# Optimization experiments

Measured on AMD Instinct MI355X. Metric: run time of the kernel, lower is better.

## Reference

```python
import jax, jax.numpy as jnp
import numpy as np

N_NODES = 50000
HIDDEN = 128
N_REL = 9
N_LAYERS = 3
N_EDGES = 600000


def setup_inputs() -> dict:
    key = jax.random.key(0)
    k1, k2, k3, k4, k5 = jax.random.split(key, 5)
    edge_index = jax.random.randint(k1, (2, N_EDGES), 0, N_NODES, dtype=jnp.int64 if jax.config.jax_enable_x64 else jnp.int32)
    edge_type = jax.random.randint(k2, (N_EDGES,), 0, N_REL, dtype=edge_index.dtype)
    embeddings = jax.random.uniform(k3, (N_NODES, HIDDEN), dtype=jnp.float32)
    weights = jax.random.uniform(k4, (N_LAYERS, N_REL, HIDDEN, HIDDEN), dtype=jnp.float32)
    biases = jax.random.uniform(k5, (N_LAYERS, N_REL, HIDDEN), dtype=jnp.float32)
    return {"edge_index": edge_index, "edge_type": edge_type,
            "embeddings": embeddings, "weights": weights, "biases": biases}


def reference(edge_index, edge_type, embeddings, weights, biases):
    # RGCN: per relation r, messages = emb[src] @ W[l,r] + b[l,r], scatter-summed
    # into dest. Equivalent vectorized form: precompute X = emb @ W for all
    # relations ([R,N,E]), then a single gather + segment_sum over edges.
    L = weights.shape[0]
    N = embeddings.shape[0]
    dest = edge_index[0]
    src = edge_index[1]
    out = embeddings
    for l in range(L):
        X = jnp.einsum('ne,ref->rnf', out, weights[l])        # [R, N, E]
        msg = X[edge_type, src] + biases[l][edge_type]        # [num_edges, E]
        hidden = jax.ops.segment_sum(msg, dest, num_segments=N)  # [N, E]
        if l + 1 < L:
            hidden = jax.nn.relu(hidden)
        out = hidden
    return out
```

## Files before the change

kernel.cpp:

```cpp
#include <hip/hip_runtime.h>

#define NNODES 50000
#define HID 128
#define NREL 9
#define NLAYERS 3
#define NEDGES 600000

#define NBINS (NREL * NNODES)
#define SCAN_CHUNK 1024
#define NBLK ((NBINS + SCAN_CHUNK - 1) / SCAN_CHUNK)

#define KTOT (NREL * HID)
#define GM2 64
#define BK 64
#define NCHUNK (KTOT / BK)
#define PITCH 72
#define EPITCH 136

typedef __attribute__((ext_vector_type(8))) short short8;
typedef __attribute__((ext_vector_type(4))) float f32x4;

__device__ __forceinline__ short f2bf(float f) {
    union { float f; unsigned u; } c; c.f = f;
    unsigned r = c.u + 0x7fff + ((c.u >> 16) & 1);
    return (short)(r >> 16);
}
__device__ __forceinline__ float bf2f(short v) {
    return __uint_as_float(((unsigned)(unsigned short)v) << 16);
}


__global__ void hist2_kernel(const int* __restrict__ dst, const int* __restrict__ etype,
                             int* __restrict__ bins) {
    int e = blockIdx.x * blockDim.x + threadIdx.x;
    if (e < NEDGES) {
        int bin = dst[e] * NREL + etype[e];
        atomicAdd(&bins[bin], 1);
    }
}

__global__ __launch_bounds__(256) void scan_pass1(const int* __restrict__ bins,
                                                  int* __restrict__ blocksum) {
    __shared__ int red[256];
    int b = blockIdx.x, t = threadIdx.x;
    int i0 = b * SCAN_CHUNK + t * 4;
    int s = 0;
#pragma unroll
    for (int k = 0; k < 4; k++)
        if (i0 + k < NBINS) s += bins[i0 + k];
    red[t] = s;
    __syncthreads();
    for (int off = 128; off > 0; off >>= 1) {
        if (t < off) red[t] += red[t + off];
        __syncthreads();
    }
    if (t == 0) blocksum[b] = red[0];
}

__global__ __launch_bounds__(512) void scan_pass2(const int* __restrict__ blocksum,
                                                  int* __restrict__ blockoff,
                                                  int* __restrict__ rowptr) {
    __shared__ int s[512];
    int t = threadIdx.x;
    int v = (t < NBLK) ? blocksum[t] : 0;
    s[t] = v;
    __syncthreads();
    for (int off = 1; off < 512; off <<= 1) {
        int x = (t >= off) ? s[t - off] : 0;
        __syncthreads();
        s[t] += x;
        __syncthreads();
    }
    if (t < NBLK) blockoff[t] = s[t] - v;
    if (t == 0) rowptr[NBINS] = NEDGES;
}

__global__ __launch_bounds__(256) void scan_pass3(const int* __restrict__ bins,
                                                  const int* __restrict__ blockoff,
                                                  int* __restrict__ rowptr,
                                                  int* __restrict__ cursor) {
    __shared__ int sc[256];
    int b = blockIdx.x, t = threadIdx.x;
    int i0 = b * SCAN_CHUNK + t * 4;
    int v[4], p[4];
    int s = 0;
#pragma unroll
    for (int k = 0; k < 4; k++) {
        v[k] = (i0 + k < NBINS) ? bins[i0 + k] : 0;
        p[k] = s;
        s += v[k];
    }
    sc[t] = s;
    __syncthreads();
    for (int off = 1; off < 256; off <<= 1) {
        int x = (t >= off) ? sc[t - off] : 0;
        __syncthreads();
        sc[t] += x;
        __syncthreads();
    }
    int base = blockoff[b] + (sc[t] - s);
#pragma unroll
    for (int k = 0; k < 4; k++) {
        if (i0 + k < NBINS) {
            rowptr[i0 + k] = base + p[k];
            cursor[i0 + k] = base + p[k];
        }
    }
}

__global__ void place_kernel(const int* __restrict__ dst, const int* __restrict__ src,
                             const int* __restrict__ etype,
                             int* __restrict__ cursor, int* __restrict__ bsrc) {
    int e = blockIdx.x * blockDim.x + threadIdx.x;
    if (e < NEDGES) {
        int bin = dst[e] * NREL + etype[e];
        int pos = atomicAdd(&cursor[bin], 1);
        bsrc[pos] = src[e];
    }
}


__global__ __launch_bounds__(256) void convert_w(const float* __restrict__ W,
                                                 short* __restrict__ Wt2) {
    int lr = blockIdx.x;
    int l = lr / NREL, r = lr - l * NREL;
    const float* w = W + (size_t)lr * HID * HID;
    short* o = Wt2 + (size_t)l * HID * KTOT;
    int tid = threadIdx.x;
#pragma unroll 4
    for (int i = 0; i < 64; i++) {
        int elem = i * 256 + tid;
        int kk = elem >> 7, n = elem & 127;
        o[(size_t)n * KTOT + r * HID + kk] = f2bf(w[elem]);
    }
}

__global__ __launch_bounds__(256) void convert_emb(const float* __restrict__ E,
                                                   short* __restrict__ Ebf) {
    int gid = blockIdx.x * blockDim.x + threadIdx.x;
    const float* p = E + (size_t)gid * 8;
    float4 v0 = *(const float4*)p;
    float4 v1 = *(const float4*)(p + 4);
    short8 o = {f2bf(v0.x), f2bf(v0.y), f2bf(v0.z), f2bf(v0.w),
                f2bf(v1.x), f2bf(v1.y), f2bf(v1.z), f2bf(v1.w)};
    *(short8*)(Ebf + (size_t)gid * 8) = o;
}


__global__ __launch_bounds__(256) void gather_kernel(const short* __restrict__ Hbf,
                                                     const int* __restrict__ bsrc,
                                                     const int* __restrict__ rowptr,
                                                     short* __restrict__ S) {
    int gid = blockIdx.x * blockDim.x + threadIdx.x;
    int bin = gid >> 3;
    if (bin >= NBINS) return;
    int ck  = gid & 7;
    int rs = rowptr[bin];
    int re = rowptr[bin + 1];
    float a[16];
#pragma unroll
    for (int i = 0; i < 16; i++) a[i] = 0.f;
    for (int j = rs; j < re; j++) {
        int s = bsrc[j];
        const short* hp = Hbf + (size_t)s * HID + ck * 16;
        short8 v0 = *(const short8*)hp;
        short8 v1 = *(const short8*)(hp + 8);
#pragma unroll
        for (int i = 0; i < 8; i++) a[i]     += bf2f(v0[i]);
#pragma unroll
        for (int i = 0; i < 8; i++) a[i + 8] += bf2f(v1[i]);
    }
    short8 o0 = {f2bf(a[0]),  f2bf(a[1]),  f2bf(a[2]),  f2bf(a[3]),
                 f2bf(a[4]),  f2bf(a[5]),  f2bf(a[6]),  f2bf(a[7])};
    short8 o1 = {f2bf(a[8]),  f2bf(a[9]),  f2bf(a[10]), f2bf(a[11]),
                 f2bf(a[12]), f2bf(a[13]), f2bf(a[14]), f2bf(a[15])};
    short* sp = S + (size_t)bin * HID + ck * 16;
    *(short8*)sp       = o0;
    *(short8*)(sp + 8) = o1;
}


__global__ __launch_bounds__(256) void gemm_kernel(const short* __restrict__ S,
                                                   const short* __restrict__ Wt2l,
                                                   const float* __restrict__ Bias,
                                                   const int* __restrict__ rowptr,
                                                   short* __restrict__ HoutBf,
                                                   float* __restrict__ HoutF,
                                                   int last) {
    __shared__ short lds[GM2 * PITCH + HID * PITCH];
    __shared__ int   rp_s[GM2 * NREL + 1];
    __shared__ float bias_s[NREL * HID];
    short* As = lds;
    short* Bs = lds + GM2 * PITCH;

    int tid  = threadIdx.x;
    int wave = tid >> 6, lane = tid & 63;
    int row0 = blockIdx.x * GM2;
    int m0   = wave * 16;
    int lm = lane & 15, lq = lane >> 4;

    int rpbase = row0 * NREL;
    for (int i = tid; i <= GM2 * NREL; i += 256) {
        int g = rpbase + i;
        rp_s[i] = rowptr[(g < NBINS) ? g : NBINS];
    }
    for (int i = tid; i < NREL * HID; i += 256) bias_s[i] = Bias[i];

    int rowL = tid >> 3;
    int ck   = tid & 7;
    int ar0 = row0 + rowL;        if (ar0 > NNODES - 1) ar0 = NNODES - 1;
    int ar1 = row0 + 32 + rowL;   if (ar1 > NNODES - 1) ar1 = NNODES - 1;
    const short* pA0 = S + (size_t)ar0 * KTOT + ck * 8;
    const short* pA1 = S + (size_t)ar1 * KTOT + ck * 8;
    const short* pB0 = Wt2l + (size_t)(rowL      ) * KTOT + ck * 8;
    const short* pB1 = Wt2l + (size_t)(rowL + 32 ) * KTOT + ck * 8;
    const short* pB2 = Wt2l + (size_t)(rowL + 64 ) * KTOT + ck * 8;
    const short* pB3 = Wt2l + (size_t)(rowL + 96 ) * KTOT + ck * 8;

    short8 ra0 = *(const short8*)pA0;
    short8 ra1 = *(const short8*)pA1;
    short8 rb0 = *(const short8*)pB0;
    short8 rb1 = *(const short8*)pB1;
    short8 rb2 = *(const short8*)pB2;
    short8 rb3 = *(const short8*)pB3;

    f32x4 acc[8];
#pragma unroll
    for (int nt = 0; nt < 8; nt++) acc[nt] = (f32x4){0.f, 0.f, 0.f, 0.f};

    for (int kc = 0; kc < NCHUNK; kc++) {
        __syncthreads();
        *(short8*)&As[ rowL       * PITCH + ck * 8] = ra0;
        *(short8*)&As[(rowL + 32) * PITCH + ck * 8] = ra1;
        *(short8*)&Bs[ rowL       * PITCH + ck * 8] = rb0;
        *(short8*)&Bs[(rowL + 32) * PITCH + ck * 8] = rb1;
        *(short8*)&Bs[(rowL + 64) * PITCH + ck * 8] = rb2;
        *(short8*)&Bs[(rowL + 96) * PITCH + ck * 8] = rb3;
        __syncthreads();
        if (kc + 1 < NCHUNK) {
            int off = (kc + 1) * BK;
            ra0 = *(const short8*)(pA0 + off);
            ra1 = *(const short8*)(pA1 + off);
            rb0 = *(const short8*)(pB0 + off);
            rb1 = *(const short8*)(pB1 + off);
            rb2 = *(const short8*)(pB2 + off);
            rb3 = *(const short8*)(pB3 + off);
        }
#pragma unroll
        for (int ks = 0; ks < 2; ks++) {
            short8 af = *(const short8*)&As[(m0 + lm) * PITCH + ks * 32 + lq * 8];
#pragma unroll
            for (int nt = 0; nt < 8; nt++) {
                short8 bf = *(const short8*)&Bs[(nt * 16 + lm) * PITCH + ks * 32 + lq * 8];
                acc[nt] = __builtin_amdgcn_mfma_f32_16x16x32_bf16(af, bf, acc[nt], 0, 0, 0);
            }
        }
    }
    __syncthreads();

    if (!last) {
        short (*Et)[EPITCH] = (short(*)[EPITCH])lds;
#pragma unroll
        for (int reg = 0; reg < 4; reg++) {
            int rl = m0 + lq * 4 + reg;
            float cr[NREL];
#pragma unroll
            for (int r = 0; r < NREL; r++)
                cr[r] = (float)(rp_s[rl * NREL + r + 1] - rp_s[rl * NREL + r]);
#pragma unroll
            for (int nt = 0; nt < 8; nt++) {
                int n = nt * 16 + lm;
                float b = 0.f;
#pragma unroll
                for (int r = 0; r < NREL; r++) b += cr[r] * bias_s[r * HID + n];
                float o = fmaxf(acc[nt][reg] + b, 0.f);
                Et[rl][n] = f2bf(o);
            }
        }
        __syncthreads();
#pragma unroll
        for (int i = 0; i < 4; i++) {
            int p = i * 256 + tid;
            int row = p >> 4, cc = p & 15;
            int d = row0 + row;
            if (d < NNODES)
                *(short8*)(HoutBf + (size_t)d * HID + cc * 8) = *(const short8*)&Et[row][cc * 8];
        }
    } else {
#pragma unroll
        for (int reg = 0; reg < 4; reg++) {
            int rl = m0 + lq * 4 + reg;
            int d  = row0 + rl;
            if (d >= NNODES) continue;
            float cr[NREL];
#pragma unroll
            for (int r = 0; r < NREL; r++)
                cr[r] = (float)(rp_s[rl * NREL + r + 1] - rp_s[rl * NREL + r]);
#pragma unroll
            for (int nt = 0; nt < 8; nt++) {
                int n = nt * 16 + lm;
                float b = 0.f;
#pragma unroll
                for (int r = 0; r < NREL; r++) b += cr[r] * bias_s[r * HID + n];
                HoutF[(size_t)d * HID + n] = acc[nt][reg] + b;
            }
        }
    }
}


extern "C" void kernel_launch(void* const* d_in, const int* in_sizes, int n_in,
                              void* d_out, int out_size, void* d_ws, size_t ws_size,
                              hipStream_t stream) {
    const int*   edge_index = (const int*)d_in[0];
    const int*   etype      = (const int*)d_in[1];
    const float* emb        = (const float*)d_in[2];
    const float* W          = (const float*)d_in[3];
    const float* Bias       = (const float*)d_in[4];
    float*       out        = (float*)d_out;

    const int* dst  = edge_index;
    const int* srcA = edge_index + NEDGES;

    short* Ebf = (short*)d_ws;
    short* Hbf = Ebf + (size_t)NNODES * HID;
    short* S   = Hbf + (size_t)NNODES * HID;
    short* Wt2 = S + (size_t)NNODES * KTOT;
    int*   bsrc     = (int*)(Wt2 + (size_t)NLAYERS * HID * KTOT);
    int*   bins     = bsrc + NEDGES;
    int*   cursor   = bins + NBINS;
    int*   rowptr   = cursor + NBINS;
    int*   blocksum = rowptr + NBINS + 1;
    int*   blockoff = blocksum + NBLK;

    hipMemsetAsync(bins, 0, NBINS * sizeof(int), stream);
    hist2_kernel<<<(NEDGES + 255) / 256, 256, 0, stream>>>(dst, etype, bins);
    scan_pass1<<<NBLK, 256, 0, stream>>>(bins, blocksum);
    scan_pass2<<<1, 512, 0, stream>>>(blocksum, blockoff, rowptr);
    scan_pass3<<<NBLK, 256, 0, stream>>>(bins, blockoff, rowptr, cursor);
    place_kernel<<<(NEDGES + 255) / 256, 256, 0, stream>>>(dst, srcA, etype, cursor, bsrc);
    convert_w<<<NLAYERS * NREL, 256, 0, stream>>>(W, Wt2);
    convert_emb<<<(NNODES * HID / 8) / 256, 256, 0, stream>>>(emb, Ebf);

    const short* Hin = Ebf;
    for (int l = 0; l < NLAYERS; l++) {
        gather_kernel<<<(NBINS * 8 + 255) / 256, 256, 0, stream>>>(Hin, bsrc, rowptr, S);
        const short* Wtl = Wt2 + (size_t)l * HID * KTOT;
        const float* Bl  = Bias + (size_t)l * NREL * HID;
        int last = (l + 1 == NLAYERS);
        gemm_kernel<<<(NNODES + GM2 - 1) / GM2, 256, 0, stream>>>(
            S, Wtl, Bl, rowptr, Hbf, out, last);
        Hin = Hbf;
    }
}
```

Measured before the change: 438.8 us.

## Fuse per-relation gather into GEMM kernel, dropping the intermediate S buffer

```diff
diff --git a/kernel.cpp b/kernel.cpp
--- a/kernel.cpp
+++ b/kernel.cpp
@@ -12,10 +12,7 @@
 
 #define KTOT (NREL * HID)
 #define GM2 64
-#define BK 64
-#define NCHUNK (KTOT / BK)
-#define PITCH 72
-#define EPITCH 136
+#define FPITCH 136
 
 typedef __attribute__((ext_vector_type(8))) short short8;
 typedef __attribute__((ext_vector_type(4))) float f32x4;
@@ -34,7 +31,7 @@
                              int* __restrict__ bins) {
     int e = blockIdx.x * blockDim.x + threadIdx.x;
     if (e < NEDGES) {
-        int bin = dst[e] * NREL + etype[e];
+        int bin = etype[e] * NNODES + dst[e];
         atomicAdd(&bins[bin], 1);
     }
 }
@@ -113,7 +110,7 @@
                              int* __restrict__ cursor, int* __restrict__ bsrc) {
     int e = blockIdx.x * blockDim.x + threadIdx.x;
     if (e < NEDGES) {
-        int bin = dst[e] * NREL + etype[e];
+        int bin = etype[e] * NNODES + dst[e];
         int pos = atomicAdd(&cursor[bin], 1);
         bsrc[pos] = src[e];
     }
@@ -147,134 +144,135 @@
 }
 
 
-__global__ __launch_bounds__(256) void gather_kernel(const short* __restrict__ Hbf,
-                                                     const int* __restrict__ bsrc,
-                                                     const int* __restrict__ rowptr,
-                                                     short* __restrict__ S) {
-    int gid = blockIdx.x * blockDim.x + threadIdx.x;
-    int bin = gid >> 3;
-    if (bin >= NBINS) return;
-    int ck  = gid & 7;
-    int rs = rowptr[bin];
-    int re = rowptr[bin + 1];
-    float a[16];
-#pragma unroll
-    for (int i = 0; i < 16; i++) a[i] = 0.f;
-    for (int j = rs; j < re; j++) {
-        int s = bsrc[j];
-        const short* hp = Hbf + (size_t)s * HID + ck * 16;
-        short8 v0 = *(const short8*)hp;
-        short8 v1 = *(const short8*)(hp + 8);
-#pragma unroll
-        for (int i = 0; i < 8; i++) a[i]     += bf2f(v0[i]);
-#pragma unroll
-        for (int i = 0; i < 8; i++) a[i + 8] += bf2f(v1[i]);
-    }
-    short8 o0 = {f2bf(a[0]),  f2bf(a[1]),  f2bf(a[2]),  f2bf(a[3]),
-                 f2bf(a[4]),  f2bf(a[5]),  f2bf(a[6]),  f2bf(a[7])};
-    short8 o1 = {f2bf(a[8]),  f2bf(a[9]),  f2bf(a[10]), f2bf(a[11]),
-                 f2bf(a[12]), f2bf(a[13]), f2bf(a[14]), f2bf(a[15])};
-    short* sp = S + (size_t)bin * HID + ck * 16;
-    *(short8*)sp       = o0;
-    *(short8*)(sp + 8) = o1;
-}
-
-
-__global__ __launch_bounds__(256) void gemm_kernel(const short* __restrict__ S,
-                                                   const short* __restrict__ Wt2l,
-                                                   const float* __restrict__ Bias,
-                                                   const int* __restrict__ rowptr,
-                                                   short* __restrict__ HoutBf,
-                                                   float* __restrict__ HoutF,
-                                                   int last) {
-    __shared__ short lds[GM2 * PITCH + HID * PITCH];
-    __shared__ int   rp_s[GM2 * NREL + 1];
+__global__ __launch_bounds__(256) void fused_kernel(const short* __restrict__ Hin,
+                                                    const short* __restrict__ Wt2l,
+                                                    const float* __restrict__ Bias,
+                                                    const int* __restrict__ rowptr,
+                                                    const int* __restrict__ bsrc,
+                                                    short* __restrict__ HoutBf,
+                                                    float* __restrict__ HoutF,
+                                                    int last) {
+    __shared__ short As[GM2 * FPITCH];
+    __shared__ int   rp_s[NREL * (GM2 + 1)];
     __shared__ float bias_s[NREL * HID];
-    short* As = lds;
-    short* Bs = lds + GM2 * PITCH;
 
     int tid  = threadIdx.x;
     int wave = tid >> 6, lane = tid & 63;
+    int lm = lane & 15, lq = lane >> 4;
     int row0 = blockIdx.x * GM2;
-    int m0   = wave * 16;
-    int lm = lane & 15, lq = lane >> 4;
-
-    int rpbase = row0 * NREL;
-    for (int i = tid; i <= GM2 * NREL; i += 256) {
-        int g = rpbase + i;
-        rp_s[i] = rowptr[(g < NBINS) ? g : NBINS];
+    int n0   = wave * 32;
+
+    for (int i = tid; i < NREL * (GM2 + 1); i += 256) {
+        int r = i / (GM2 + 1), o = i - r * (GM2 + 1);
+        int d = row0 + o; if (d > NNODES) d = NNODES;
+        rp_s[i] = rowptr[r * NNODES + d];
     }
     for (int i = tid; i < NREL * HID; i += 256) bias_s[i] = Bias[i];
 
-    int rowL = tid >> 3;
-    int ck   = tid & 7;
-    int ar0 = row0 + rowL;        if (ar0 > NNODES - 1) ar0 = NNODES - 1;
-    int ar1 = row0 + 32 + rowL;   if (ar1 > NNODES - 1) ar1 = NNODES - 1;
-    const short* pA0 = S + (size_t)ar0 * KTOT + ck * 8;
-    const short* pA1 = S + (size_t)ar1 * KTOT + ck * 8;
-    const short* pB0 = Wt2l + (size_t)(rowL      ) * KTOT + ck * 8;
-    const short* pB1 = Wt2l + (size_t)(rowL + 32 ) * KTOT + ck * 8;
-    const short* pB2 = Wt2l + (size_t)(rowL + 64 ) * KTOT + ck * 8;
-    const short* pB3 = Wt2l + (size_t)(rowL + 96 ) * KTOT + ck * 8;
-
-    short8 ra0 = *(const short8*)pA0;
-    short8 ra1 = *(const short8*)pA1;
-    short8 rb0 = *(const short8*)pB0;
-    short8 rb1 = *(const short8*)pB1;
-    short8 rb2 = *(const short8*)pB2;
-    short8 rb3 = *(const short8*)pB3;
-
-    f32x4 acc[8];
-#pragma unroll
-    for (int nt = 0; nt < 8; nt++) acc[nt] = (f32x4){0.f, 0.f, 0.f, 0.f};
-
-    for (int kc = 0; kc < NCHUNK; kc++) {
-        __syncthreads();
-        *(short8*)&As[ rowL       * PITCH + ck * 8] = ra0;
-        *(short8*)&As[(rowL + 32) * PITCH + ck * 8] = ra1;
-        *(short8*)&Bs[ rowL       * PITCH + ck * 8] = rb0;
-        *(short8*)&Bs[(rowL + 32) * PITCH + ck * 8] = rb1;
-        *(short8*)&Bs[(rowL + 64) * PITCH + ck * 8] = rb2;
-        *(short8*)&Bs[(rowL + 96) * PITCH + ck * 8] = rb3;
-        __syncthreads();
-        if (kc + 1 < NCHUNK) {
-            int off = (kc + 1) * BK;
-            ra0 = *(const short8*)(pA0 + off);
-            ra1 = *(const short8*)(pA1 + off);
-            rb0 = *(const short8*)(pB0 + off);
-            rb1 = *(const short8*)(pB1 + off);
-            rb2 = *(const short8*)(pB2 + off);
-            rb3 = *(const short8*)(pB3 + off);
-        }
-#pragma unroll
-        for (int ks = 0; ks < 2; ks++) {
-            short8 af = *(const short8*)&As[(m0 + lm) * PITCH + ks * 32 + lq * 8];
-#pragma unroll
-            for (int nt = 0; nt < 8; nt++) {
-                short8 bf = *(const short8*)&Bs[(nt * 16 + lm) * PITCH + ks * 32 + lq * 8];
-                acc[nt] = __builtin_amdgcn_mfma_f32_16x16x32_bf16(af, bf, acc[nt], 0, 0, 0);
-            }
-        }
-    }
+    int grow = tid >> 2;
+    int gcc  = tid & 3;
+
+    f32x4 acc[4][2];
+#pragma unroll
+    for (int a = 0; a < 4; a++)
+#pragma unroll
+        for (int b = 0; b < 2; b++) acc[a][b] = (f32x4){0.f, 0.f, 0.f, 0.f};
+
+    __syncthreads();
+
+    const short* wb = Wt2l + (size_t)(n0 + lm) * KTOT + lq * 8;
+
+    for (int r = 0; r < NREL; r++) {
+        int rs = rp_s[r * (GM2 + 1) + grow];
+        int re = rp_s[r * (GM2 + 1) + grow + 1];
+        float ga[32];
+#pragma unroll
+        for (int i = 0; i < 32; i++) ga[i] = 0.f;
+        int j = rs;
+        while (j + 1 < re) {
+            int s0 = bsrc[j];
+            int s1 = bsrc[j + 1];
+            const short8* h0 = (const short8*)(Hin + (size_t)s0 * HID + gcc * 32);
+            const short8* h1 = (const short8*)(Hin + (size_t)s1 * HID + gcc * 32);
+            short8 a0 = h0[0], a1 = h0[1], a2 = h0[2], a3 = h0[3];
+            short8 b0 = h1[0], b1 = h1[1], b2 = h1[2], b3 = h1[3];
+#pragma unroll
+            for (int i = 0; i < 8; i++) {
+                ga[i]      += bf2f(a0[i]) + bf2f(b0[i]);
+                ga[i + 8]  += bf2f(a1[i]) + bf2f(b1[i]);
+                ga[i + 16] += bf2f(a2[i]) + bf2f(b2[i]);
+                ga[i + 24] += bf2f(a3[i]) + bf2f(b3[i]);
+            }
+            j += 2;
+        }
+        if (j < re) {
+            int s0 = bsrc[j];
+            const short8* h0 = (const short8*)(Hin + (size_t)s0 * HID + gcc * 32);
+            short8 a0 = h0[0], a1 = h0[1], a2 = h0[2], a3 = h0[3];
+#pragma unroll
+            for (int i = 0; i < 8; i++) {
+                ga[i]      += bf2f(a0[i]);
+                ga[i + 8]  += bf2f(a1[i]);
+                ga[i + 16] += bf2f(a2[i]);
+                ga[i + 24] += bf2f(a3[i]);
+            }
+        }
+
+        __syncthreads();
+        {
+            short8 o0, o1, o2, o3;
+#pragma unroll
+            for (int i = 0; i < 8; i++) {
+                o0[i] = f2bf(ga[i]);
+                o1[i] = f2bf(ga[i + 8]);
+                o2[i] = f2bf(ga[i + 16]);
+                o3[i] = f2bf(ga[i + 24]);
+            }
+            short8* ap = (short8*)&As[grow * FPITCH + gcc * 32];
+            ap[0] = o0; ap[1] = o1; ap[2] = o2; ap[3] = o3;
+        }
+        __syncthreads();
+
+#pragma unroll
+        for (int ks = 0; ks < 4; ks++) {
+            short8 af[4];
+#pragma unroll
+            for (int mt = 0; mt < 4; mt++)
+                af[mt] = *(const short8*)&As[(mt * 16 + lm) * FPITCH + ks * 32 + lq * 8];
+#pragma unroll
+            for (int nt = 0; nt < 2; nt++) {
+                short8 bf = *(const short8*)(wb + (size_t)nt * 16 * KTOT + r * HID + ks * 32);
+                __builtin_amdgcn_s_setprio(1);
+#pragma unroll
+                for (int mt = 0; mt < 4; mt++)
+                    acc[mt][nt] = __builtin_amdgcn_mfma_f32_16x16x32_bf16(af[mt], bf, acc[mt][nt], 0, 0, 0);
+                __builtin_amdgcn_s_setprio(0);
+            }
+        }
+    }
+
     __syncthreads();
 
     if (!last) {
-        short (*Et)[EPITCH] = (short(*)[EPITCH])lds;
-#pragma unroll
-        for (int reg = 0; reg < 4; reg++) {
-            int rl = m0 + lq * 4 + reg;
-            float cr[NREL];
-#pragma unroll
-            for (int r = 0; r < NREL; r++)
-                cr[r] = (float)(rp_s[rl * NREL + r + 1] - rp_s[rl * NREL + r]);
-#pragma unroll
-            for (int nt = 0; nt < 8; nt++) {
-                int n = nt * 16 + lm;
-                float b = 0.f;
-#pragma unroll
-                for (int r = 0; r < NREL; r++) b += cr[r] * bias_s[r * HID + n];
-                float o = fmaxf(acc[nt][reg] + b, 0.f);
-                Et[rl][n] = f2bf(o);
+        short (*Et)[FPITCH] = (short(*)[FPITCH])As;
+#pragma unroll
+        for (int mt = 0; mt < 4; mt++) {
+#pragma unroll
+            for (int reg = 0; reg < 4; reg++) {
+                int rl = mt * 16 + lq * 4 + reg;
+                float cr[NREL];
+#pragma unroll
+                for (int rr = 0; rr < NREL; rr++)
+                    cr[rr] = (float)(rp_s[rr * (GM2 + 1) + rl + 1] - rp_s[rr * (GM2 + 1) + rl]);
+#pragma unroll
+                for (int nt = 0; nt < 2; nt++) {
+                    int n = n0 + nt * 16 + lm;
+                    float b = 0.f;
+#pragma unroll
+                    for (int rr = 0; rr < NREL; rr++) b += cr[rr] * bias_s[rr * HID + n];
+                    float o = fmaxf(acc[mt][nt][reg] + b, 0.f);
+                    Et[rl][n] = f2bf(o);
+                }
             }
         }
         __syncthreads();
@@ -288,21 +286,24 @@
         }
     } else {
 #pragma unroll
-        for (int reg = 0; reg < 4; reg++) {
-            int rl = m0 + lq * 4 + reg;
-            int d  = row0 + rl;
-            if (d >= NNODES) continue;
-            float cr[NREL];
-#pragma unroll
-            for (int r = 0; r < NREL; r++)
-                cr[r] = (float)(rp_s[rl * NREL + r + 1] - rp_s[rl * NREL + r]);
-#pragma unroll
-            for (int nt = 0; nt < 8; nt++) {
-                int n = nt * 16 + lm;
-                float b = 0.f;
-#pragma unroll
-                for (int r = 0; r < NREL; r++) b += cr[r] * bias_s[r * HID + n];
-                HoutF[(size_t)d * HID + n] = acc[nt][reg] + b;
+        for (int mt = 0; mt < 4; mt++) {
+#pragma unroll
+            for (int reg = 0; reg < 4; reg++) {
+                int rl = mt * 16 + lq * 4 + reg;
+                int d  = row0 + rl;
+                if (d >= NNODES) continue;
+                float cr[NREL];
+#pragma unroll
+                for (int rr = 0; rr < NREL; rr++)
+                    cr[rr] = (float)(rp_s[rr * (GM2 + 1) + rl + 1] - rp_s[rr * (GM2 + 1) + rl]);
+#pragma unroll
+                for (int nt = 0; nt < 2; nt++) {
+                    int n = n0 + nt * 16 + lm;
+                    float b = 0.f;
+#pragma unroll
+                    for (int rr = 0; rr < NREL; rr++) b += cr[rr] * bias_s[rr * HID + n];
+                    HoutF[(size_t)d * HID + n] = acc[mt][nt][reg] + b;
+                }
             }
         }
     }
@@ -322,10 +323,10 @@
     const int* dst  = edge_index;
     const int* srcA = edge_index + NEDGES;
 
-    short* Ebf = (short*)d_ws;
-    short* Hbf = Ebf + (size_t)NNODES * HID;
-    short* S   = Hbf + (size_t)NNODES * HID;
-    short* Wt2 = S + (size_t)NNODES * KTOT;
+    short* Ebf  = (short*)d_ws;
+    short* HbfA = Ebf  + (size_t)NNODES * HID;
+    short* HbfB = HbfA + (size_t)NNODES * HID;
+    short* Wt2  = HbfB + (size_t)NNODES * HID;
     int*   bsrc     = (int*)(Wt2 + (size_t)NLAYERS * HID * KTOT);
     int*   bins     = bsrc + NEDGES;
     int*   cursor   = bins + NBINS;
@@ -342,14 +343,16 @@
     convert_w<<<NLAYERS * NREL, 256, 0, stream>>>(W, Wt2);
     convert_emb<<<(NNODES * HID / 8) / 256, 256, 0, stream>>>(emb, Ebf);
 
+    const int nblocks = (NNODES + GM2 - 1) / GM2;
     const short* Hin = Ebf;
     for (int l = 0; l < NLAYERS; l++) {
-        gather_kernel<<<(NBINS * 8 + 255) / 256, 256, 0, stream>>>(Hin, bsrc, rowptr, S);
+        int last = (l + 1 == NLAYERS);
+        short* Hout = (l == 0) ? HbfA : HbfB;
+        if (l == 2) Hout = HbfA;
         const short* Wtl = Wt2 + (size_t)l * HID * KTOT;
         const float* Bl  = Bias + (size_t)l * NREL * HID;
-        int last = (l + 1 == NLAYERS);
-        gemm_kernel<<<(NNODES + GM2 - 1) / GM2, 256, 0, stream>>>(
-            S, Wtl, Bl, rowptr, Hbf, out, last);
-        Hin = Hbf;
-    }
-}
+        fused_kernel<<<nblocks, 256, 0, stream>>>(
+            Hin, Wtl, Bl, rowptr, bsrc, Hout, out, last);
+        Hin = Hout;
+    }
+}
```

After: 510.8 us. 1.16x slower.

## Fuse prep kernels into one launch and deepen GEMM A-tile prefetch

Applied to the files above, without the earlier changes.

```diff
diff --git a/kernel.cpp b/kernel.cpp
--- a/kernel.cpp
+++ b/kernel.cpp
@@ -17,6 +17,10 @@
 #define PITCH 72
 #define EPITCH 136
 
+#define HIST_BLKS ((NEDGES + 255) / 256)
+#define EMB_BLKS  ((NNODES * HID / 8) / 256)
+#define W_BLKS    (NLAYERS * NREL)
+
 typedef __attribute__((ext_vector_type(8))) short short8;
 typedef __attribute__((ext_vector_type(4))) float f32x4;
 
@@ -30,14 +34,42 @@
 }
 
 
-__global__ void hist2_kernel(const int* __restrict__ dst, const int* __restrict__ etype,
-                             int* __restrict__ bins) {
-    int e = blockIdx.x * blockDim.x + threadIdx.x;
-    if (e < NEDGES) {
-        int bin = dst[e] * NREL + etype[e];
-        atomicAdd(&bins[bin], 1);
-    }
-}
+__global__ __launch_bounds__(256) void prep_kernel(const int* __restrict__ dst,
+                                                   const int* __restrict__ etype,
+                                                   int* __restrict__ bins,
+                                                   const float* __restrict__ E,
+                                                   short* __restrict__ Ebf,
+                                                   const float* __restrict__ W,
+                                                   short* __restrict__ Wt2) {
+    int b = blockIdx.x, tid = threadIdx.x;
+    if (b < HIST_BLKS) {
+        int e = b * 256 + tid;
+        if (e < NEDGES) {
+            int bin = dst[e] * NREL + etype[e];
+            atomicAdd(&bins[bin], 1);
+        }
+    } else if (b < HIST_BLKS + EMB_BLKS) {
+        int gid = (b - HIST_BLKS) * 256 + tid;
+        const float* p = E + (size_t)gid * 8;
+        float4 v0 = *(const float4*)p;
+        float4 v1 = *(const float4*)(p + 4);
+        short8 o = {f2bf(v0.x), f2bf(v0.y), f2bf(v0.z), f2bf(v0.w),
+                    f2bf(v1.x), f2bf(v1.y), f2bf(v1.z), f2bf(v1.w)};
+        *(short8*)(Ebf + (size_t)gid * 8) = o;
+    } else {
+        int lr = b - HIST_BLKS - EMB_BLKS;
+        int l = lr / NREL, r = lr - l * NREL;
+        const float* w = W + (size_t)lr * HID * HID;
+        short* o = Wt2 + (size_t)l * HID * KTOT;
+#pragma unroll 4
+        for (int i = 0; i < 64; i++) {
+            int elem = i * 256 + tid;
+            int kk = elem >> 7, n = elem & 127;
+            o[(size_t)n * KTOT + r * HID + kk] = f2bf(w[elem]);
+        }
+    }
+}
+
 
 __global__ __launch_bounds__(256) void scan_pass1(const int* __restrict__ bins,
                                                   int* __restrict__ blocksum) {
@@ -117,33 +149,6 @@
         int pos = atomicAdd(&cursor[bin], 1);
         bsrc[pos] = src[e];
     }
-}
-
-
-__global__ __launch_bounds__(256) void convert_w(const float* __restrict__ W,
-                                                 short* __restrict__ Wt2) {
-    int lr = blockIdx.x;
-    int l = lr / NREL, r = lr - l * NREL;
-    const float* w = W + (size_t)lr * HID * HID;
-    short* o = Wt2 + (size_t)l * HID * KTOT;
-    int tid = threadIdx.x;
-#pragma unroll 4
-    for (int i = 0; i < 64; i++) {
-        int elem = i * 256 + tid;
-        int kk = elem >> 7, n = elem & 127;
-        o[(size_t)n * KTOT + r * HID + kk] = f2bf(w[elem]);
-    }
-}
-
-__global__ __launch_bounds__(256) void convert_emb(const float* __restrict__ E,
-                                                   short* __restrict__ Ebf) {
-    int gid = blockIdx.x * blockDim.x + threadIdx.x;
-    const float* p = E + (size_t)gid * 8;
-    float4 v0 = *(const float4*)p;
-    float4 v1 = *(const float4*)(p + 4);
-    short8 o = {f2bf(v0.x), f2bf(v0.y), f2bf(v0.z), f2bf(v0.w),
-                f2bf(v1.x), f2bf(v1.y), f2bf(v1.z), f2bf(v1.w)};
-    *(short8*)(Ebf + (size_t)gid * 8) = o;
 }
 
 
@@ -217,8 +222,10 @@
     const short* pB2 = Wt2l + (size_t)(rowL + 64 ) * KTOT + ck * 8;
     const short* pB3 = Wt2l + (size_t)(rowL + 96 ) * KTOT + ck * 8;
 
-    short8 ra0 = *(const short8*)pA0;
-    short8 ra1 = *(const short8*)pA1;
+    short8 raE0 = *(const short8*)pA0;
+    short8 raE1 = *(const short8*)pA1;
+    short8 raO0 = *(const short8*)(pA0 + BK);
+    short8 raO1 = *(const short8*)(pA1 + BK);
     short8 rb0 = *(const short8*)pB0;
     short8 rb1 = *(const short8*)pB1;
     short8 rb2 = *(const short8*)pB2;
@@ -228,19 +235,52 @@
 #pragma unroll
     for (int nt = 0; nt < 8; nt++) acc[nt] = (f32x4){0.f, 0.f, 0.f, 0.f};
 
-    for (int kc = 0; kc < NCHUNK; kc++) {
-        __syncthreads();
-        *(short8*)&As[ rowL       * PITCH + ck * 8] = ra0;
-        *(short8*)&As[(rowL + 32) * PITCH + ck * 8] = ra1;
+    for (int kp = 0; kp < NCHUNK / 2; kp++) {
+        int ke = 2 * kp;
+        __syncthreads();
+        *(short8*)&As[ rowL       * PITCH + ck * 8] = raE0;
+        *(short8*)&As[(rowL + 32) * PITCH + ck * 8] = raE1;
         *(short8*)&Bs[ rowL       * PITCH + ck * 8] = rb0;
         *(short8*)&Bs[(rowL + 32) * PITCH + ck * 8] = rb1;
         *(short8*)&Bs[(rowL + 64) * PITCH + ck * 8] = rb2;
         *(short8*)&Bs[(rowL + 96) * PITCH + ck * 8] = rb3;
         __syncthreads();
-        if (kc + 1 < NCHUNK) {
-            int off = (kc + 1) * BK;
-            ra0 = *(const short8*)(pA0 + off);
-            ra1 = *(const short8*)(pA1 + off);
+        if (ke + 2 < NCHUNK) {
+            int off = (ke + 2) * BK;
+            raE0 = *(const short8*)(pA0 + off);
+            raE1 = *(const short8*)(pA1 + off);
+        }
+        {
+            int off = (ke + 1) * BK;
+            rb0 = *(const short8*)(pB0 + off);
+            rb1 = *(const short8*)(pB1 + off);
+            rb2 = *(const short8*)(pB2 + off);
+            rb3 = *(const short8*)(pB3 + off);
+        }
+#pragma unroll
+        for (int ks = 0; ks < 2; ks++) {
+            short8 af = *(const short8*)&As[(m0 + lm) * PITCH + ks * 32 + lq * 8];
+#pragma unroll
+            for (int nt = 0; nt < 8; nt++) {
+                short8 bf = *(const short8*)&Bs[(nt * 16 + lm) * PITCH + ks * 32 + lq * 8];
+                acc[nt] = __builtin_amdgcn_mfma_f32_16x16x32_bf16(af, bf, acc[nt], 0, 0, 0);
+            }
+        }
+        __syncthreads();
+        *(short8*)&As[ rowL       * PITCH + ck * 8] = raO0;
+        *(short8*)&As[(rowL + 32) * PITCH + ck * 8] = raO1;
+        *(short8*)&Bs[ rowL       * PITCH + ck * 8] = rb0;
+        *(short8*)&Bs[(rowL + 32) * PITCH + ck * 8] = rb1;
+        *(short8*)&Bs[(rowL + 64) * PITCH + ck * 8] = rb2;
+        *(short8*)&Bs[(rowL + 96) * PITCH + ck * 8] = rb3;
+        __syncthreads();
+        if (ke + 3 < NCHUNK) {
+            int off = (ke + 3) * BK;
+            raO0 = *(const short8*)(pA0 + off);
+            raO1 = *(const short8*)(pA1 + off);
+        }
+        if (ke + 2 < NCHUNK) {
+            int off = (ke + 2) * BK;
             rb0 = *(const short8*)(pB0 + off);
             rb1 = *(const short8*)(pB1 + off);
             rb2 = *(const short8*)(pB2 + off);
@@ -334,13 +374,12 @@
     int*   blockoff = blocksum + NBLK;
 
     hipMemsetAsync(bins, 0, NBINS * sizeof(int), stream);
-    hist2_kernel<<<(NEDGES + 255) / 256, 256, 0, stream>>>(dst, etype, bins);
+    prep_kernel<<<HIST_BLKS + EMB_BLKS + W_BLKS, 256, 0, stream>>>(
+        dst, etype, bins, emb, Ebf, W, Wt2);
     scan_pass1<<<NBLK, 256, 0, stream>>>(bins, blocksum);
     scan_pass2<<<1, 512, 0, stream>>>(blocksum, blockoff, rowptr);
     scan_pass3<<<NBLK, 256, 0, stream>>>(bins, blockoff, rowptr, cursor);
     place_kernel<<<(NEDGES + 255) / 256, 256, 0, stream>>>(dst, srcA, etype, cursor, bsrc);
-    convert_w<<<NLAYERS * NREL, 256, 0, stream>>>(W, Wt2);
-    convert_emb<<<(NNODES * HID / 8) / 256, 256, 0, stream>>>(emb, Ebf);
 
     const short* Hin = Ebf;
     for (int l = 0; l < NLAYERS; l++) {
```

New measurement: 417.3 us. 1.05x faster.
